# Performance work log

Hardware: AMD Instinct MI355X
Metric: run time of the kernel (lower is better)

Reference implementation:

```python
import jax, jax.numpy as jnp
import numpy as np

N = 100000
E = 1600000
H = 128       # hidden_channels
HEADS = 8
HD = H // HEADS  # head_dim = 16


def setup_inputs() -> dict:
    key = jax.random.key(0)
    ks = jax.random.split(key, 10)
    x = jax.random.normal(ks[0], (N, H), dtype=jnp.float32)
    gap_edge_index = jax.random.randint(ks[1], (2, E), 0, N, dtype=jnp.int64)
    s = 1.0 / np.sqrt(H)
    Wq = jax.random.normal(ks[2], (H, H), dtype=jnp.float32) * s
    bq = jnp.zeros((H,), dtype=jnp.float32)
    Wk = jax.random.normal(ks[3], (H, H), dtype=jnp.float32) * s
    bk = jnp.zeros((H,), dtype=jnp.float32)
    Wv = jax.random.normal(ks[4], (H, H), dtype=jnp.float32) * s
    bv = jnp.zeros((H,), dtype=jnp.float32)
    Wo = jax.random.normal(ks[5], (H, H), dtype=jnp.float32) * s
    bo = jnp.zeros((H,), dtype=jnp.float32)
    return {"x": x, "gap_edge_index": gap_edge_index,
            "Wq": Wq, "bq": bq, "Wk": Wk, "bk": bk,
            "Wv": Wv, "bv": bv, "Wo": Wo, "bo": bo}


def reference(x, gap_edge_index, Wq, bq, Wk, bk, Wv, bv, Wo, bo):
    n = x.shape[0]
    q = (x @ Wq + bq).reshape(n, HEADS, HD)
    k = (x @ Wk + bk).reshape(n, HEADS, HD)
    v = (x @ Wv + bv).reshape(n, HEADS, HD)
    src, dst = gap_edge_index[0], gap_edge_index[1]
    # per-edge, per-head scores: [E, heads]
    scores = jnp.einsum('ehd,ehd->eh', q[dst], k[src]) / jnp.sqrt(jnp.float32(HD))
    # NOTE: original softmaxes over ALL edges (dim=0), not per-dst segment
    w = jax.nn.softmax(scores, axis=0)
    # scatter-add weighted v[src] into dst: [N, heads, head_dim]
    attended = jax.ops.segment_sum(w[:, :, None] * v[src], dst, num_segments=n)
    attended = attended.reshape(n, HEADS * HD)
    return x + attended @ Wo + bo
```

## Files before the change

### kernel.cpp

```cpp
#include <hip/hip_runtime.h>
#include <cstdint>
#include <cstddef>

#define N_NODES 100000
#define E_EDGES 1600000
#define HCH 128
#define NHEADS 8
#define HDIM 16

typedef unsigned int uint;
typedef unsigned short ushort;
typedef unsigned char uchar;
typedef __attribute__((ext_vector_type(8))) short short8;
typedef __attribute__((ext_vector_type(4))) float floatx4;
typedef __attribute__((ext_vector_type(2))) float floatx2;

constexpr int GTILES = (N_NODES + 63) / 64;

__device__ __forceinline__ ushort f2bf(float f) {
    uint u = __float_as_uint(f);
    u = (u + 0x7fff + ((u >> 16) & 1)) >> 16;
    return (ushort)u;
}
__device__ __forceinline__ float bflo(uint p) { return __uint_as_float(p << 16); }
__device__ __forceinline__ float bfhi(uint p) { return __uint_as_float(p & 0xffff0000u); }

constexpr int BSHIFT = 8;
constexpr int NBUCK  = ((N_NODES - 1) >> BSHIFT) + 1;
constexpr int S1_GRID = 256;
constexpr int S1_CH   = (E_EDGES + S1_GRID - 1) / S1_GRID;
constexpr int S2_CAP  = 6144;
constexpr int FU_BLOCKS = 2048;
constexpr int FU_GROUPS = FU_BLOCKS * 16;
constexpr int GQ_BLOCKS = 1278;
constexpr int GQ_STRIDE = 426;
constexpr int GO_BLOCKS = 1024;

__global__ __launch_bounds__(256) void prep_hist(
    const float* __restrict__ Wq, const float* __restrict__ Wk,
    const float* __restrict__ Wv, const float* __restrict__ Wo,
    ushort* __restrict__ wall,
    const int* __restrict__ dst, int* __restrict__ bucket_total)
{
    const int t = threadIdx.x;
    const int bid = blockIdx.x;
    if (bid < S1_GRID) {
        __shared__ int cnt[NBUCK];
        for (int b = t; b < NBUCK; b += 256) cnt[b] = 0;
        __syncthreads();
        const int e0 = bid * S1_CH;
        const int n = min(S1_CH, E_EDGES - e0);
        for (int i = t; i < n; i += 256)
            atomicAdd(&cnt[dst[e0 + i] >> BSHIFT], 1);
        __syncthreads();
        for (int b = t; b < NBUCK; b += 256)
            if (cnt[b]) atomicAdd(&bucket_total[b], cnt[b]);
        return;
    }
    int r = (bid - S1_GRID) * 16 + (t >> 4);
    int k0 = (t & 15) * 8;
    const float* W;
    if (r < 128)      W = Wq;
    else if (r < 256) W = Wk;
    else if (r < 384) W = Wv;
    else              W = Wo;
    int n = r & 127;
    uint4 u;
    u.x = (uint)f2bf(W[(size_t)(k0 + 0) * HCH + n]) | ((uint)f2bf(W[(size_t)(k0 + 1) * HCH + n]) << 16);
    u.y = (uint)f2bf(W[(size_t)(k0 + 2) * HCH + n]) | ((uint)f2bf(W[(size_t)(k0 + 3) * HCH + n]) << 16);
    u.z = (uint)f2bf(W[(size_t)(k0 + 4) * HCH + n]) | ((uint)f2bf(W[(size_t)(k0 + 5) * HCH + n]) << 16);
    u.w = (uint)f2bf(W[(size_t)(k0 + 6) * HCH + n]) | ((uint)f2bf(W[(size_t)(k0 + 7) * HCH + n]) << 16);
    *(uint4*)(wall + (size_t)r * HCH + k0) = u;
}

__global__ __launch_bounds__(512) void bucket_scan(
    const int* __restrict__ bucket_total, int* __restrict__ bucket_start,
    int* __restrict__ bucket_cursor, int* __restrict__ offsets)
{
    __shared__ int s[512];
    const int t = threadIdx.x;
    int v = (t < NBUCK) ? bucket_total[t] : 0;
    s[t] = v;
    __syncthreads();
    for (int off = 1; off < 512; off <<= 1) {
        int a = (t >= off) ? s[t - off] : 0;
        __syncthreads();
        s[t] += a;
        __syncthreads();
    }
    int excl = s[t] - v;
    if (t < NBUCK) { bucket_start[t] = excl; bucket_cursor[t] = excl; }
    if (t == 0) { bucket_start[NBUCK] = E_EDGES; offsets[N_NODES] = E_EDGES; }
}

__global__ __launch_bounds__(256) void mega_qkv_scatter(
    const float* __restrict__ A, const ushort* __restrict__ wall,
    const float* __restrict__ bq, const float* __restrict__ bk, const float* __restrict__ bv,
    uchar* __restrict__ qe, uchar* __restrict__ kb, uchar* __restrict__ vb,
    const int* __restrict__ src, const int* __restrict__ dst,
    int* __restrict__ bucket_cursor, uint* __restrict__ tmp,
    int M)
{
    __shared__ __align__(16) char sm[34816];
    const int t = threadIdx.x;
    const int bid = blockIdx.x;

    if (bid < S1_GRID) {
        int* cnt = (int*)sm;
        for (int b = t; b < NBUCK; b += 256) cnt[b] = 0;
        __syncthreads();
        const int e0 = bid * S1_CH;
        const int n = min(S1_CH, E_EDGES - e0);
        for (int i = t; i < n; i += 256)
            atomicAdd(&cnt[dst[e0 + i] >> BSHIFT], 1);
        __syncthreads();
        for (int b = t; b < NBUCK; b += 256) {
            int c = cnt[b];
            cnt[b] = c ? atomicAdd(&bucket_cursor[b], c) : 0;
        }
        __syncthreads();
        for (int i = t; i < n; i += 256) {
            int d = dst[e0 + i];
            int s = src[e0 + i];
            int pos = atomicAdd(&cnt[d >> BSHIFT], 1);
            tmp[pos] = (uint)s | ((uint)(d & 255) << 24);
        }
        return;
    }

    ushort (*As)[136] = (ushort(*)[136])sm;
    ushort (*Cs)[136] = (ushort(*)[136])(sm + 17408);

    const int b = bid - S1_GRID;
    const int mode = b % 3;
    const int tile0 = b / 3;
    const float* bias;
    uchar* outp;
    if (mode == 0)      { bias = bq; outp = qe; }
    else if (mode == 1) { bias = bk; outp = kb; }
    else                { bias = bv; outp = vb; }

    const int lane = t & 63;
    const int w = t >> 6;
    const int m_l = lane & 15;
    const int q_l = lane >> 4;

    short8 wfr[2][4];
    {
        const ushort* wb = wall + (size_t)(mode * 128 + 2 * w * 16 + m_l) * HCH + q_l * 8;
#pragma unroll
        for (int tlj = 0; tlj < 2; tlj++)
#pragma unroll
            for (int ks = 0; ks < 4; ks++)
                wfr[tlj][ks] = *(const short8*)(wb + (size_t)tlj * 16 * HCH + ks * 32);
    }

    const int eu = t & 15;
    const float4 eb0 = *(const float4*)(bias + eu * 8);
    const float4 eb1 = *(const float4*)(bias + eu * 8 + 4);
    const int arow = t >> 5, ac4 = t & 31;

    float4 a4[8];
    {
        const int mb = tile0 * 64;
#pragma unroll
        for (int i = 0; i < 8; i++) {
            int g = mb + arow + i * 8;
            a4[i] = make_float4(0.f, 0.f, 0.f, 0.f);
            if (g < M) a4[i] = *(const float4*)(A + (size_t)g * HCH + ac4 * 4);
        }
    }

    for (int tile = tile0; tile < GTILES; tile += GQ_STRIDE) {
        const int mb = tile * 64;
#pragma unroll
        for (int i = 0; i < 8; i++) {
            uint lo = (uint)f2bf(a4[i].x) | ((uint)f2bf(a4[i].y) << 16);
            uint hi = (uint)f2bf(a4[i].z) | ((uint)f2bf(a4[i].w) << 16);
            *(uint2*)(&As[arow + i * 8][ac4 * 4]) = make_uint2(lo, hi);
        }
        const int ntile = tile + GQ_STRIDE;
        if (ntile < GTILES) {
            const int nmb = ntile * 64;
#pragma unroll
            for (int i = 0; i < 8; i++) {
                int g = nmb + arow + i * 8;
                float4 v = make_float4(0.f, 0.f, 0.f, 0.f);
                if (g < M) v = *(const float4*)(A + (size_t)g * HCH + ac4 * 4);
                a4[i] = v;
            }
        }
        __syncthreads();

        floatx4 acc[4][2];
#pragma unroll
        for (int ms = 0; ms < 4; ms++) {
            acc[ms][0] = (floatx4){0.f, 0.f, 0.f, 0.f};
            acc[ms][1] = (floatx4){0.f, 0.f, 0.f, 0.f};
        }
#pragma unroll
        for (int ks = 0; ks < 4; ks++) {
#pragma unroll
            for (int ms = 0; ms < 4; ms++) {
                short8 af = *(const short8*)(&As[ms * 16 + m_l][ks * 32 + q_l * 8]);
                acc[ms][0] = __builtin_amdgcn_mfma_f32_16x16x32_bf16(af, wfr[0][ks], acc[ms][0], 0, 0, 0);
                acc[ms][1] = __builtin_amdgcn_mfma_f32_16x16x32_bf16(af, wfr[1][ks], acc[ms][1], 0, 0, 0);
            }
        }
#pragma unroll
        for (int ms = 0; ms < 4; ms++)
#pragma unroll
            for (int tlj = 0; tlj < 2; tlj++)
#pragma unroll
                for (int r = 0; r < 4; r++)
                    Cs[ms * 16 + q_l * 4 + r][(2 * w + tlj) * 16 + m_l] = f2bf(acc[ms][tlj][r]);
        __syncthreads();

#pragma unroll
        for (int i = 0; i < 4; i++) {
            int row = (t >> 4) + i * 16;
            int g = mb + row;
            if (g < M) {
                uint4 c = *(const uint4*)(&Cs[row][eu * 8]);
                int r0 = __builtin_amdgcn_cvt_pk_fp8_f32(bflo(c.x) + eb0.x, bfhi(c.x) + eb0.y, 0, false);
                r0 = __builtin_amdgcn_cvt_pk_fp8_f32(bflo(c.y) + eb0.z, bfhi(c.y) + eb0.w, r0, true);
                int r1 = __builtin_amdgcn_cvt_pk_fp8_f32(bflo(c.z) + eb1.x, bfhi(c.z) + eb1.y, 0, false);
                r1 = __builtin_amdgcn_cvt_pk_fp8_f32(bflo(c.w) + eb1.z, bfhi(c.w) + eb1.w, r1, true);
                *(uint2*)(outp + (size_t)g * 128 + eu * 8) = make_uint2((uint)r0, (uint)r1);
            }
        }
        __syncthreads();
    }
}

__global__ __launch_bounds__(256) void sort_scatter2(
    const uint* __restrict__ tmp, const int* __restrict__ bucket_start,
    int* __restrict__ psrc, int* __restrict__ offsets)
{
    __shared__ uint le[S2_CAP];
    __shared__ int cnt[256];
    __shared__ int s[256];
    __shared__ int cur[256];
    const int t = threadIdx.x;
    const int b = blockIdx.x;
    const int bstart = bucket_start[b];
    const int n = bucket_start[b + 1] - bstart;
    cnt[t] = 0;
    __syncthreads();
    for (int i = t; i < n; i += 256) {
        uint e = tmp[bstart + i];
        if (i < S2_CAP) le[i] = e;
        atomicAdd(&cnt[e >> 24], 1);
    }
    __syncthreads();
    int v = cnt[t];
    s[t] = v;
    __syncthreads();
    for (int off = 1; off < 256; off <<= 1) {
        int a = (t >= off) ? s[t - off] : 0;
        __syncthreads();
        s[t] += a;
        __syncthreads();
    }
    int excl = s[t] - v;
    int node = (b << BSHIFT) + t;
    if (node < N_NODES) offsets[node] = bstart + excl;
    cur[t] = excl;
    __syncthreads();
    for (int i = t; i < n; i += 256) {
        uint e = (i < S2_CAP) ? le[i] : tmp[bstart + i];
        int pos = bstart + atomicAdd(&cur[e >> 24], 1);
        psrc[pos] = (int)(e & 0x1FFFFu);
    }
}

__device__ __forceinline__ float edge_w(
    uint2 e, floatx2 q0, floatx2 q1, floatx2 q2, floatx2 q3)
{
    floatx2 dp = q0 * __builtin_amdgcn_cvt_pk_f32_fp8((int)e.x, false);
    dp += q1 * __builtin_amdgcn_cvt_pk_f32_fp8((int)e.x, true);
    dp += q2 * __builtin_amdgcn_cvt_pk_f32_fp8((int)e.y, false);
    dp += q3 * __builtin_amdgcn_cvt_pk_f32_fp8((int)e.y, true);
    float p = dp.x + dp.y;
    p += __shfl_xor(p, 1);
    return __expf(p * 0.25f - 2.772588722f);
}
__device__ __forceinline__ void edge_acc(
    uint2 e, float wgt, floatx2& a01, floatx2& a23, floatx2& a45, floatx2& a67)
{
    floatx2 wv = {wgt, wgt};
    a01 += wv * __builtin_amdgcn_cvt_pk_f32_fp8((int)e.x, false);
    a23 += wv * __builtin_amdgcn_cvt_pk_f32_fp8((int)e.x, true);
    a45 += wv * __builtin_amdgcn_cvt_pk_f32_fp8((int)e.y, false);
    a67 += wv * __builtin_amdgcn_cvt_pk_f32_fp8((int)e.y, true);
}

#define LOADQ(S, base) do { \
    int jj1 = min((base) + 1, end - 1); \
    int jj2 = min((base) + 2, end - 1); \
    int jj3 = min((base) + 3, end - 1); \
    int u0 = psrc[(base)], u1 = psrc[jj1], u2 = psrc[jj2], u3 = psrc[jj3]; \
    k##S##0 = *(const uint2*)(kb + (size_t)u0 * 128 + sub * 8); \
    k##S##1 = *(const uint2*)(kb + (size_t)u1 * 128 + sub * 8); \
    k##S##2 = *(const uint2*)(kb + (size_t)u2 * 128 + sub * 8); \
    k##S##3 = *(const uint2*)(kb + (size_t)u3 * 128 + sub * 8); \
    v##S##0 = *(const uint2*)(vb + (size_t)u0 * 128 + sub * 8); \
    v##S##1 = *(const uint2*)(vb + (size_t)u1 * 128 + sub * 8); \
    v##S##2 = *(const uint2*)(vb + (size_t)u2 * 128 + sub * 8); \
    v##S##3 = *(const uint2*)(vb + (size_t)u3 * 128 + sub * 8); \
} while (0)

#define COMPQ(S, base) do { \
    float w0 = edge_w(k##S##0, q0, q1, q2, q3); \
    float w1 = edge_w(k##S##1, q0, q1, q2, q3); \
    float w2 = edge_w(k##S##2, q0, q1, q2, q3); \
    float w3 = edge_w(k##S##3, q0, q1, q2, q3); \
    if ((base) + 1 >= end) w1 = 0.f; \
    if ((base) + 2 >= end) w2 = 0.f; \
    if ((base) + 3 >= end) w3 = 0.f; \
    lsum += w0 + w1 + w2 + w3; \
    edge_acc(v##S##0, w0, a01, a23, a45, a67); \
    edge_acc(v##S##1, w1, a01, a23, a45, a67); \
    edge_acc(v##S##2, w2, a01, a23, a45, a67); \
    edge_acc(v##S##3, w3, a01, a23, a45, a67); \
} while (0)

__global__ __launch_bounds__(256) void edge_fused(
    const uchar* __restrict__ qe, const uchar* __restrict__ kb, const uchar* __restrict__ vb,
    const int* __restrict__ psrc, const int* __restrict__ offsets,
    uchar* __restrict__ attended, float* __restrict__ block_l)
{
    const int t = threadIdx.x;
    const int sub = t & 15;
    const int gg0 = blockIdx.x * 16 + (t >> 4);

    float lsum = 0.f;

    for (int d = gg0; d < N_NODES; d += FU_GROUPS) {
        const int start = offsets[d];
        const int end   = offsets[d + 1];

        uint2 qw = *(const uint2*)(qe + (size_t)d * 128 + sub * 8);
        floatx2 q0 = __builtin_amdgcn_cvt_pk_f32_fp8((int)qw.x, false);
        floatx2 q1 = __builtin_amdgcn_cvt_pk_f32_fp8((int)qw.x, true);
        floatx2 q2 = __builtin_amdgcn_cvt_pk_f32_fp8((int)qw.y, false);
        floatx2 q3 = __builtin_amdgcn_cvt_pk_f32_fp8((int)qw.y, true);

        floatx2 a01 = {0.f, 0.f}, a23 = {0.f, 0.f}, a45 = {0.f, 0.f}, a67 = {0.f, 0.f};

        uint2 kA0, kA1, kA2, kA3, vA0, vA1, vA2, vA3;
        uint2 kB0, kB1, kB2, kB3, vB0, vB1, vB2, vB3;

        int i = start;
        if (i < end) {
            LOADQ(A, i);
            while (true) {
                if (i + 4 < end) LOADQ(B, i + 4);
                COMPQ(A, i);
                i += 4;
                if (i >= end) break;
                if (i + 4 < end) LOADQ(A, i + 4);
                COMPQ(B, i);
                i += 4;
                if (i >= end) break;
            }
        }

        int r0 = __builtin_amdgcn_cvt_pk_fp8_f32(a01.x, a01.y, 0, false);
        r0 = __builtin_amdgcn_cvt_pk_fp8_f32(a23.x, a23.y, r0, true);
        int r1 = __builtin_amdgcn_cvt_pk_fp8_f32(a45.x, a45.y, 0, false);
        r1 = __builtin_amdgcn_cvt_pk_fp8_f32(a67.x, a67.y, r1, true);
        *(uint2*)(attended + (size_t)d * 128 + sub * 8) = make_uint2((uint)r0, (uint)r1);
    }

    __shared__ float sl[256];
    sl[t] = lsum;
    __syncthreads();
    if (t < 8) {
        float L = 0.f;
        for (int base = 0; base < 256; base += 16)
            L += sl[base + 2 * t] + sl[base + 2 * t + 1];
        block_l[blockIdx.x * 8 + t] = 0.5f * L;
    }
}

__global__ __launch_bounds__(256) void gemm_out(
    const uchar* __restrict__ A, const ushort* __restrict__ wall,
    const float* __restrict__ bias, const float* __restrict__ res,
    const float* __restrict__ block_l,
    float* __restrict__ C, int M)
{
    __shared__ __align__(16) char sm[34816];
    ushort (*As)[136] = (ushort(*)[136])sm;
    ushort (*Cs)[136] = (ushort(*)[136])(sm + 17408);
    __shared__ float invl_s[8];
    __shared__ float sl[256];

    const int t = threadIdx.x;

    {
        float l = 0.f;
        for (int i = t; i < FU_BLOCKS * 8; i += 256) l += block_l[i];
        sl[t] = l;
        __syncthreads();
        if (t < 8) {
            float L = 0.f;
            for (int j = t; j < 256; j += 8) L += sl[j];
            invl_s[t] = 1.0f / L;
        }
        __syncthreads();
    }

    const int lane = t & 63;
    const int w = t >> 6;
    const int m_l = lane & 15;
    const int q_l = lane >> 4;

    short8 wfr[2][4];
    {
        const ushort* wb = wall + (size_t)(384 + 2 * w * 16 + m_l) * HCH + q_l * 8;
#pragma unroll
        for (int tlj = 0; tlj < 2; tlj++)
#pragma unroll
            for (int ks = 0; ks < 4; ks++)
                wfr[tlj][ks] = *(const short8*)(wb + (size_t)tlj * 16 * HCH + ks * 32);
    }

    const int arow = t >> 4, au = t & 15;
    const float invl_a = invl_s[au >> 1];
    const int eu = t & 31;
    const float4 eb = *(const float4*)(bias + eu * 4);

    uint2 a2[4];
    {
        const int mb = blockIdx.x * 64;
#pragma unroll
        for (int i = 0; i < 4; i++) {
            int g = mb + arow + i * 16;
            a2[i] = make_uint2(0, 0);
            if (g < M) a2[i] = *(const uint2*)(A + (size_t)g * 128 + au * 8);
        }
    }

    for (int tile = blockIdx.x; tile < GTILES; tile += GO_BLOCKS) {
        const int mb = tile * 64;
#pragma unroll
        for (int i = 0; i < 4; i++) {
            floatx2 f01 = __builtin_amdgcn_cvt_pk_f32_fp8((int)a2[i].x, false);
            floatx2 f23 = __builtin_amdgcn_cvt_pk_f32_fp8((int)a2[i].x, true);
            floatx2 f45 = __builtin_amdgcn_cvt_pk_f32_fp8((int)a2[i].y, false);
            floatx2 f67 = __builtin_amdgcn_cvt_pk_f32_fp8((int)a2[i].y, true);
            uint4 o;
            o.x = (uint)f2bf(f01.x * invl_a) | ((uint)f2bf(f01.y * invl_a) << 16);
            o.y = (uint)f2bf(f23.x * invl_a) | ((uint)f2bf(f23.y * invl_a) << 16);
            o.z = (uint)f2bf(f45.x * invl_a) | ((uint)f2bf(f45.y * invl_a) << 16);
            o.w = (uint)f2bf(f67.x * invl_a) | ((uint)f2bf(f67.y * invl_a) << 16);
            *(uint4*)(&As[arow + i * 16][au * 8]) = o;
        }
        const int ntile = tile + GO_BLOCKS;
        if (ntile < GTILES) {
            const int nmb = ntile * 64;
#pragma unroll
            for (int i = 0; i < 4; i++) {
                int g = nmb + arow + i * 16;
                uint2 v = make_uint2(0, 0);
                if (g < M) v = *(const uint2*)(A + (size_t)g * 128 + au * 8);
                a2[i] = v;
            }
        }
        __syncthreads();

        floatx4 acc[4][2];
#pragma unroll
        for (int ms = 0; ms < 4; ms++) {
            acc[ms][0] = (floatx4){0.f, 0.f, 0.f, 0.f};
            acc[ms][1] = (floatx4){0.f, 0.f, 0.f, 0.f};
        }
#pragma unroll
        for (int ks = 0; ks < 4; ks++) {
#pragma unroll
            for (int ms = 0; ms < 4; ms++) {
                short8 af = *(const short8*)(&As[ms * 16 + m_l][ks * 32 + q_l * 8]);
                acc[ms][0] = __builtin_amdgcn_mfma_f32_16x16x32_bf16(af, wfr[0][ks], acc[ms][0], 0, 0, 0);
                acc[ms][1] = __builtin_amdgcn_mfma_f32_16x16x32_bf16(af, wfr[1][ks], acc[ms][1], 0, 0, 0);
            }
        }
#pragma unroll
        for (int ms = 0; ms < 4; ms++)
#pragma unroll
            for (int tlj = 0; tlj < 2; tlj++)
#pragma unroll
                for (int r = 0; r < 4; r++)
                    Cs[ms * 16 + q_l * 4 + r][(2 * w + tlj) * 16 + m_l] = f2bf(acc[ms][tlj][r]);
        __syncthreads();

#pragma unroll
        for (int i = 0; i < 8; i++) {
            int row = (t >> 5) + i * 8;
            int g = mb + row;
            if (g < M) {
                uint2 c = *(const uint2*)(&Cs[row][eu * 4]);
                float4 r4 = *(const float4*)(res + (size_t)g * HCH + eu * 4);
                float4 o;
                o.x = bflo(c.x) + eb.x + r4.x;
                o.y = bfhi(c.x) + eb.y + r4.y;
                o.z = bflo(c.y) + eb.z + r4.z;
                o.w = bfhi(c.y) + eb.w + r4.w;
                *(float4*)(C + (size_t)g * HCH + eu * 4) = o;
            }
        }
        __syncthreads();
    }
}

extern "C" void kernel_launch(void* const* d_in, const int* in_sizes, int n_in,
                              void* d_out, int out_size, void* d_ws, size_t ws_size,
                              hipStream_t stream)
{
    const float* x  = (const float*)d_in[0];
    const int* eidx = (const int*)d_in[1];
    const float* Wq = (const float*)d_in[2];
    const float* bq = (const float*)d_in[3];
    const float* Wk = (const float*)d_in[4];
    const float* bk = (const float*)d_in[5];
    const float* Wv = (const float*)d_in[6];
    const float* bv = (const float*)d_in[7];
    const float* Wo = (const float*)d_in[8];
    const float* bo = (const float*)d_in[9];
    float* out = (float*)d_out;

    char* ws = (char*)d_ws;
    constexpr size_t SZ_F8  = (size_t)N_NODES * HCH;
    constexpr size_t SZ_PS  = (size_t)E_EDGES * sizeof(int);
    constexpr size_t SZ_TMP = (size_t)E_EDGES * sizeof(uint);
    size_t off = 0;
    uchar* qe = (uchar*)(ws + off); off += SZ_F8;
    uchar* kb = (uchar*)(ws + off); off += SZ_F8;
    uchar* vb = (uchar*)(ws + off); off += SZ_F8;
    uchar* attended = (uchar*)(ws + off); off += SZ_F8;
    int*    psrc     = (int*)(ws + off);    off += SZ_PS;
    uint*   tmp      = (uint*)(ws + off);   off += SZ_TMP;
    int*    offsets  = (int*)(ws + off);    off += ((size_t)N_NODES + 1) * 4 + 8;
    int*    bucket_total  = (int*)(ws + off); off += (NBUCK + 1) * 4;
    int*    bucket_start  = (int*)(ws + off); off += (NBUCK + 1) * 4;
    int*    bucket_cursor = (int*)(ws + off); off += (NBUCK + 1) * 4;
    float*  block_l   = (float*)(ws + off); off += (size_t)FU_BLOCKS * 8 * sizeof(float);
    ushort* wall = (ushort*)(ws + off); off += (size_t)512 * HCH * 2;
    const int* src = eidx;
    const int* dst = eidx + E_EDGES;

    dim3 blk(256);

    hipMemsetAsync(bucket_total, 0, (NBUCK + 1) * 4, stream);
    prep_hist<<<S1_GRID + 32, blk, 0, stream>>>(Wq, Wk, Wv, Wo, wall, dst, bucket_total);
    bucket_scan<<<1, 512, 0, stream>>>(bucket_total, bucket_start, bucket_cursor, offsets);

    mega_qkv_scatter<<<S1_GRID + GQ_BLOCKS, blk, 0, stream>>>(
        x, wall, bq, bk, bv, qe, kb, vb, src, dst, bucket_cursor, tmp, N_NODES);

    sort_scatter2<<<NBUCK, blk, 0, stream>>>(tmp, bucket_start, psrc, offsets);

    edge_fused<<<FU_BLOCKS, blk, 0, stream>>>(qe, kb, vb, psrc, offsets, attended, block_l);

    gemm_out<<<GO_BLOCKS, blk, 0, stream>>>(attended, wall, bo, x, block_l, out, N_NODES);
}
```

Measured before the change: 292.7 us.

## Compute Q, K, V per tile in one block and atomically reduce softmax sums

Each QKV block now loads its A tile once and runs all three projections (Q, K, V) against it, swapping weight fragments between two register sets. Before, each of three blocks reloaded and reconverted the same A tile for only one projection. Separately, edge_fused now atomically adds its per-head softmax denominators into 8 global floats. This replaces the per-block array that every gemm_out block had to re-reduce. The costs are extra weight loads per tile, higher register pressure, and 8-address atomic contention across 2048 blocks.

```diff
diff --git a/kernel.cpp b/kernel.cpp
--- a/kernel.cpp
+++ b/kernel.cpp
@@ -32,8 +32,7 @@
 constexpr int S2_CAP  = 6144;
 constexpr int FU_BLOCKS = 2048;
 constexpr int FU_GROUPS = FU_BLOCKS * 16;
-constexpr int GQ_BLOCKS = 1278;
-constexpr int GQ_STRIDE = 426;
+constexpr int GQ_BLOCKS = 1024;
 constexpr int GO_BLOCKS = 1024;
 
 __global__ __launch_bounds__(256) void prep_hist(
@@ -93,6 +92,57 @@
     if (t == 0) { bucket_start[NBUCK] = E_EDGES; offsets[N_NODES] = E_EDGES; }
 }
 
+#define LOADW(R, mode_) do { \
+    const ushort* wb_ = wall + (size_t)((mode_) * 128 + 2 * w * 16 + m_l) * HCH + q_l * 8; \
+    _Pragma("unroll") \
+    for (int tlj = 0; tlj < 2; tlj++) \
+        _Pragma("unroll") \
+        for (int ks = 0; ks < 4; ks++) \
+            R[tlj][ks] = *(const short8*)(wb_ + (size_t)tlj * 16 * HCH + ks * 32); \
+} while (0)
+
+#define GEMM_EPI(R, outp_, bias_) do { \
+    floatx4 acc[4][2]; \
+    _Pragma("unroll") \
+    for (int ms = 0; ms < 4; ms++) { \
+        acc[ms][0] = (floatx4){0.f, 0.f, 0.f, 0.f}; \
+        acc[ms][1] = (floatx4){0.f, 0.f, 0.f, 0.f}; \
+    } \
+    _Pragma("unroll") \
+    for (int ks = 0; ks < 4; ks++) { \
+        _Pragma("unroll") \
+        for (int ms = 0; ms < 4; ms++) { \
+            short8 af = *(const short8*)(&As[ms * 16 + m_l][ks * 32 + q_l * 8]); \
+            acc[ms][0] = __builtin_amdgcn_mfma_f32_16x16x32_bf16(af, R[0][ks], acc[ms][0], 0, 0, 0); \
+            acc[ms][1] = __builtin_amdgcn_mfma_f32_16x16x32_bf16(af, R[1][ks], acc[ms][1], 0, 0, 0); \
+        } \
+    } \
+    _Pragma("unroll") \
+    for (int ms = 0; ms < 4; ms++) \
+        _Pragma("unroll") \
+        for (int tlj = 0; tlj < 2; tlj++) \
+            _Pragma("unroll") \
+            for (int r = 0; r < 4; r++) \
+                Cs[ms * 16 + q_l * 4 + r][(2 * w + tlj) * 16 + m_l] = f2bf(acc[ms][tlj][r]); \
+    __syncthreads(); \
+    _Pragma("unroll") \
+    for (int i = 0; i < 4; i++) { \
+        int row = (t >> 4) + i * 16; \
+        int g = mb + row; \
+        if (g < M) { \
+            uint4 c = *(const uint4*)(&Cs[row][eu * 8]); \
+            float4 b0 = *(const float4*)((bias_) + eu * 8); \
+            float4 b1 = *(const float4*)((bias_) + eu * 8 + 4); \
+            int r0 = __builtin_amdgcn_cvt_pk_fp8_f32(bflo(c.x) + b0.x, bfhi(c.x) + b0.y, 0, false); \
+            r0 = __builtin_amdgcn_cvt_pk_fp8_f32(bflo(c.y) + b0.z, bfhi(c.y) + b0.w, r0, true); \
+            int r1 = __builtin_amdgcn_cvt_pk_fp8_f32(bflo(c.z) + b1.x, bfhi(c.z) + b1.y, 0, false); \
+            r1 = __builtin_amdgcn_cvt_pk_fp8_f32(bflo(c.w) + b1.z, bfhi(c.w) + b1.w, r1, true); \
+            *(uint2*)((outp_) + (size_t)g * 128 + eu * 8) = make_uint2((uint)r0, (uint)r1); \
+        } \
+    } \
+    __syncthreads(); \
+} while (0)
+
 __global__ __launch_bounds__(256) void mega_qkv_scatter(
     const float* __restrict__ A, const ushort* __restrict__ wall,
     const float* __restrict__ bq, const float* __restrict__ bk, const float* __restrict__ bv,
@@ -132,37 +182,18 @@
     ushort (*Cs)[136] = (ushort(*)[136])(sm + 17408);
 
     const int b = bid - S1_GRID;
-    const int mode = b % 3;
-    const int tile0 = b / 3;
-    const float* bias;
-    uchar* outp;
-    if (mode == 0)      { bias = bq; outp = qe; }
-    else if (mode == 1) { bias = bk; outp = kb; }
-    else                { bias = bv; outp = vb; }
-
     const int lane = t & 63;
     const int w = t >> 6;
     const int m_l = lane & 15;
     const int q_l = lane >> 4;
-
-    short8 wfr[2][4];
-    {
-        const ushort* wb = wall + (size_t)(mode * 128 + 2 * w * 16 + m_l) * HCH + q_l * 8;
-#pragma unroll
-        for (int tlj = 0; tlj < 2; tlj++)
-#pragma unroll
-            for (int ks = 0; ks < 4; ks++)
-                wfr[tlj][ks] = *(const short8*)(wb + (size_t)tlj * 16 * HCH + ks * 32);
-    }
-
     const int eu = t & 15;
-    const float4 eb0 = *(const float4*)(bias + eu * 8);
-    const float4 eb1 = *(const float4*)(bias + eu * 8 + 4);
     const int arow = t >> 5, ac4 = t & 31;
+
+    short8 wA[2][4], wB[2][4];
 
     float4 a4[8];
     {
-        const int mb = tile0 * 64;
+        const int mb = b * 64;
 #pragma unroll
         for (int i = 0; i < 8; i++) {
             int g = mb + arow + i * 8;
@@ -171,15 +202,16 @@
         }
     }
 
-    for (int tile = tile0; tile < GTILES; tile += GQ_STRIDE) {
+    for (int tile = b; tile < GTILES; tile += GQ_BLOCKS) {
         const int mb = tile * 64;
+        LOADW(wA, 0);
 #pragma unroll
         for (int i = 0; i < 8; i++) {
             uint lo = (uint)f2bf(a4[i].x) | ((uint)f2bf(a4[i].y) << 16);
             uint hi = (uint)f2bf(a4[i].z) | ((uint)f2bf(a4[i].w) << 16);
             *(uint2*)(&As[arow + i * 8][ac4 * 4]) = make_uint2(lo, hi);
         }
-        const int ntile = tile + GQ_STRIDE;
+        const int ntile = tile + GQ_BLOCKS;
         if (ntile < GTILES) {
             const int nmb = ntile * 64;
 #pragma unroll
@@ -192,44 +224,11 @@
         }
         __syncthreads();
 
-        floatx4 acc[4][2];
-#pragma unroll
-        for (int ms = 0; ms < 4; ms++) {
-            acc[ms][0] = (floatx4){0.f, 0.f, 0.f, 0.f};
-            acc[ms][1] = (floatx4){0.f, 0.f, 0.f, 0.f};
-        }
-#pragma unroll
-        for (int ks = 0; ks < 4; ks++) {
-#pragma unroll
-            for (int ms = 0; ms < 4; ms++) {
-                short8 af = *(const short8*)(&As[ms * 16 + m_l][ks * 32 + q_l * 8]);
-                acc[ms][0] = __builtin_amdgcn_mfma_f32_16x16x32_bf16(af, wfr[0][ks], acc[ms][0], 0, 0, 0);
-                acc[ms][1] = __builtin_amdgcn_mfma_f32_16x16x32_bf16(af, wfr[1][ks], acc[ms][1], 0, 0, 0);
-            }
-        }
-#pragma unroll
-        for (int ms = 0; ms < 4; ms++)
-#pragma unroll
-            for (int tlj = 0; tlj < 2; tlj++)
-#pragma unroll
-                for (int r = 0; r < 4; r++)
-                    Cs[ms * 16 + q_l * 4 + r][(2 * w + tlj) * 16 + m_l] = f2bf(acc[ms][tlj][r]);
-        __syncthreads();
-
-#pragma unroll
-        for (int i = 0; i < 4; i++) {
-            int row = (t >> 4) + i * 16;
-            int g = mb + row;
-            if (g < M) {
-                uint4 c = *(const uint4*)(&Cs[row][eu * 8]);
-                int r0 = __builtin_amdgcn_cvt_pk_fp8_f32(bflo(c.x) + eb0.x, bfhi(c.x) + eb0.y, 0, false);
-                r0 = __builtin_amdgcn_cvt_pk_fp8_f32(bflo(c.y) + eb0.z, bfhi(c.y) + eb0.w, r0, true);
-                int r1 = __builtin_amdgcn_cvt_pk_fp8_f32(bflo(c.z) + eb1.x, bfhi(c.z) + eb1.y, 0, false);
-                r1 = __builtin_amdgcn_cvt_pk_fp8_f32(bflo(c.w) + eb1.z, bfhi(c.w) + eb1.w, r1, true);
-                *(uint2*)(outp + (size_t)g * 128 + eu * 8) = make_uint2((uint)r0, (uint)r1);
-            }
-        }
-        __syncthreads();
+        LOADW(wB, 1);
+        GEMM_EPI(wA, qe, bq);
+        LOADW(wA, 2);
+        GEMM_EPI(wB, kb, bk);
+        GEMM_EPI(wA, vb, bv);
     }
 }
 
@@ -328,7 +327,7 @@
 __global__ __launch_bounds__(256) void edge_fused(
     const uchar* __restrict__ qe, const uchar* __restrict__ kb, const uchar* __restrict__ vb,
     const int* __restrict__ psrc, const int* __restrict__ offsets,
-    uchar* __restrict__ attended, float* __restrict__ block_l)
+    uchar* __restrict__ attended, float* __restrict__ head_l)
 {
     const int t = threadIdx.x;
     const int sub = t & 15;
@@ -380,36 +379,25 @@
         float L = 0.f;
         for (int base = 0; base < 256; base += 16)
             L += sl[base + 2 * t] + sl[base + 2 * t + 1];
-        block_l[blockIdx.x * 8 + t] = 0.5f * L;
+        atomicAdd(&head_l[t], 0.5f * L);
     }
 }
 
 __global__ __launch_bounds__(256) void gemm_out(
     const uchar* __restrict__ A, const ushort* __restrict__ wall,
     const float* __restrict__ bias, const float* __restrict__ res,
-    const float* __restrict__ block_l,
+    const float* __restrict__ head_l,
     float* __restrict__ C, int M)
 {
     __shared__ __align__(16) char sm[34816];
     ushort (*As)[136] = (ushort(*)[136])sm;
     ushort (*Cs)[136] = (ushort(*)[136])(sm + 17408);
     __shared__ float invl_s[8];
-    __shared__ float sl[256];
 
     const int t = threadIdx.x;
 
-    {
-        float l = 0.f;
-        for (int i = t; i < FU_BLOCKS * 8; i += 256) l += block_l[i];
-        sl[t] = l;
-        __syncthreads();
-        if (t < 8) {
-            float L = 0.f;
-            for (int j = t; j < 256; j += 8) L += sl[j];
-            invl_s[t] = 1.0f / L;
-        }
-        __syncthreads();
-    }
+    if (t < 8) invl_s[t] = 1.0f / head_l[t];
+    __syncthreads();
 
     const int lane = t & 63;
     const int w = t >> 6;
@@ -542,16 +530,16 @@
     uint*   tmp      = (uint*)(ws + off);   off += SZ_TMP;
     int*    offsets  = (int*)(ws + off);    off += ((size_t)N_NODES + 1) * 4 + 8;
     int*    bucket_total  = (int*)(ws + off); off += (NBUCK + 1) * 4;
+    float*  head_l        = (float*)(ws + off); off += 8 * 4;
     int*    bucket_start  = (int*)(ws + off); off += (NBUCK + 1) * 4;
     int*    bucket_cursor = (int*)(ws + off); off += (NBUCK + 1) * 4;
-    float*  block_l   = (float*)(ws + off); off += (size_t)FU_BLOCKS * 8 * sizeof(float);
     ushort* wall = (ushort*)(ws + off); off += (size_t)512 * HCH * 2;
     const int* src = eidx;
     const int* dst = eidx + E_EDGES;
 
     dim3 blk(256);
 
-    hipMemsetAsync(bucket_total, 0, (NBUCK + 1) * 4, stream);
+    hipMemsetAsync(bucket_total, 0, (NBUCK + 1) * 4 + 8 * 4, stream);
     prep_hist<<<S1_GRID + 32, blk, 0, stream>>>(Wq, Wk, Wv, Wo, wall, dst, bucket_total);
     bucket_scan<<<1, 512, 0, stream>>>(bucket_total, bucket_start, bucket_cursor, offsets);
 
@@ -560,7 +548,7 @@
 
     sort_scatter2<<<NBUCK, blk, 0, stream>>>(tmp, bucket_start, psrc, offsets);
 
-    edge_fused<<<FU_BLOCKS, blk, 0, stream>>>(qe, kb, vb, psrc, offsets, attended, block_l);
-
-    gemm_out<<<GO_BLOCKS, blk, 0, stream>>>(attended, wall, bo, x, block_l, out, N_NODES);
-}
+    edge_fused<<<FU_BLOCKS, blk, 0, stream>>>(qe, kb, vb, psrc, offsets, attended, head_l);
+
+    gemm_out<<<GO_BLOCKS, blk, 0, stream>>>(attended, wall, bo, x, head_l, out, N_NODES);
+}
```

Result: faster. 281.4 us (-3.9%).
